# Kernel tuning notes

Hardware: AMD Instinct MI355X
Metric: run time of the kernel (lower is better)

The kernel has to match this reference:

```python
import jax, jax.numpy as jnp
import numpy as np

N = 50000          # nodes
E = 800000         # edges (before self-loops)
F_IN = 500         # input features
H1, C1 = 8, 16     # layer-1 heads, per-head channels
NUM_CLASSES = 7
NEG_SLOPE = 0.2


def setup_inputs() -> dict:
    key = jax.random.key(0)
    ks = jax.random.split(key, 10)
    s = 0.05
    return {
        "x": jax.random.normal(ks[0], (N, F_IN), jnp.float32),
        "edge_index": jax.random.randint(ks[1], (2, E), 0, N, dtype=jnp.int64),
        "W1": jax.random.normal(ks[2], (F_IN, H1 * C1), jnp.float32) * s,
        "att_src1": jax.random.normal(ks[3], (H1, C1), jnp.float32) * s,
        "att_dst1": jax.random.normal(ks[4], (H1, C1), jnp.float32) * s,
        "b1": jnp.zeros((H1 * C1,), jnp.float32),
        "W2": jax.random.normal(ks[5], (H1 * C1, NUM_CLASSES), jnp.float32) * s,
        "att_src2": jax.random.normal(ks[6], (1, NUM_CLASSES), jnp.float32) * s,
        "att_dst2": jax.random.normal(ks[7], (1, NUM_CLASSES), jnp.float32) * s,
        "b2": jnp.zeros((NUM_CLASSES,), jnp.float32),
    }


def _gat_conv(x, W, att_src, att_dst, bias, src, dst, concat):
    # PyG GATConv (eval mode: attention dropout is identity).
    H, C = att_src.shape
    h = (x @ W).reshape(N, H, C)                      # [N,H,C]
    a_src = jnp.sum(h * att_src, axis=-1)             # [N,H]
    a_dst = jnp.sum(h * att_dst, axis=-1)             # [N,H]
    e = a_src[src] + a_dst[dst]                       # [Et,H] per-edge logits
    e = jax.nn.leaky_relu(e, NEG_SLOPE)
    # segment softmax over incoming edges of each destination node
    m = jax.ops.segment_max(e, dst, num_segments=N)   # [N,H]
    e = jnp.exp(e - m[dst])
    denom = jax.ops.segment_sum(e, dst, num_segments=N)  # [N,H]
    alpha = e / (denom[dst] + 1e-16)                  # [Et,H]
    msg = h[src] * alpha[:, :, None]                  # [Et,H,C]
    out = jax.ops.segment_sum(msg, dst, num_segments=N)  # [N,H,C]
    if concat:
        out = out.reshape(N, H * C)
    else:
        out = out.mean(axis=1)
    return out + bias


def reference(x, edge_index, W1, att_src1, att_dst1, b1, W2, att_src2, att_dst2, b2):
    # add self-loops (PyG default add_self_loops=True)
    loops = jnp.arange(N, dtype=edge_index.dtype)
    src = jnp.concatenate([edge_index[0], loops])
    dst = jnp.concatenate([edge_index[1], loops])
    h = _gat_conv(x, W1, att_src1, att_dst1, b1, src, dst, concat=True)
    h = jax.nn.relu(h)
    # F.dropout(p=0.6, training=False) -> identity in eval mode
    out = _gat_conv(h, W2, att_src2, att_dst2, b2, src, dst, concat=False)
    return out
```

## Files before the change

kernel.cpp:

```cpp
#include <hip/hip_runtime.h>
#include <hip/hip_bf16.h>

#define NN 50000
#define EE 800000
#define ETOT 850000
#define FIN 500
#define HC 128
#define NH 8
#define CH 16
#define NC 7

#define OW1  0
#define OAS1 64000
#define OAD1 64128
#define OB1  64256
#define OW2  64384
#define OAS2 65280
#define OAD2 65287
#define OB2  65294
#define WTOT 65301

#define GR1  64
#define GK   32
#define KPAD 512
#define ASTR 40
#define BSTR 40

typedef __hip_bfloat16 bf16;
typedef __attribute__((ext_vector_type(8))) short short8;
typedef __attribute__((ext_vector_type(4))) float f32x4;

__device__ __forceinline__ float b2f(const bf16 v) { return __bfloat162float(v); }
__device__ __forceinline__ float lrelu(float v) { return fmaxf(v, 0.2f * v); }
__device__ __forceinline__ float elog(float v) { return __expf(fminf(lrelu(v), 30.f)); }
__device__ __forceinline__ float blo(unsigned w) { return __uint_as_float(w << 16); }
__device__ __forceinline__ float bhi(unsigned w) { return __uint_as_float(w & 0xffff0000u); }
__device__ __forceinline__ unsigned short f2bu(float f)
{
    bf16 h = __float2bfloat16(f);
    return *(unsigned short*)&h;
}

__device__ __forceinline__ int eread(const void* __restrict__ eidx, long long i, int is64)
{
    if (is64) return (int)((const long long*)eidx)[i];
    return ((const int*)eidx)[i];
}

__global__ void detect_kernel(const unsigned short* __restrict__ xraw,
                              const unsigned int* __restrict__ eraw,
                              int* __restrict__ flags, int* __restrict__ rowptr)
{
    __shared__ int s_insane, s_oddnz;
    if (threadIdx.x == 0) { s_insane = 0; s_oddnz = 0; }
    __syncthreads();
    int insane = 0;
    for (int i = threadIdx.x; i < 8192; i += 256) {
        const unsigned int bits = ((unsigned int)xraw[i]) << 16;
        const float v = __uint_as_float(bits);
        const float a = fabsf(v);
        const bool sane = (v == 0.0f) || (a >= 1e-30f && a <= 1e4f);
        if (!sane) insane++;
    }
    int oddnz = 0;
    for (int i = threadIdx.x; i < 512; i += 256) {
        if (eraw[2 * i + 1] != 0u) oddnz++;
    }
    atomicAdd(&s_insane, insane);
    atomicAdd(&s_oddnz, oddnz);
    __syncthreads();
    if (threadIdx.x == 0) {
        flags[0] = (s_insane < 256) ? 1 : 0;
        flags[1] = (s_oddnz == 0) ? 1 : 0;
        rowptr[NN] = ETOT;
    }
}

__global__ void conv_w_kernel(const void* W1, const void* as1, const void* ad1, const void* b1,
                              const void* W2, const void* as2, const void* ad2, const void* b2,
                              float* __restrict__ wc, const int* __restrict__ flags)
{
    const int i = blockIdx.x * blockDim.x + threadIdx.x;
    if (i >= WTOT) return;
    const void* src; int off;
    if (i < OAS1)      { src = W1;  off = i - OW1; }
    else if (i < OAD1) { src = as1; off = i - OAS1; }
    else if (i < OB1)  { src = ad1; off = i - OAD1; }
    else if (i < OW2)  { src = b1;  off = i - OB1; }
    else if (i < OAS2) { src = W2;  off = i - OW2; }
    else if (i < OAD2) { src = as2; off = i - OAS2; }
    else if (i < OB2)  { src = ad2; off = i - OAD2; }
    else               { src = b2;  off = i - OB2; }
    float v;
    if (flags[0]) v = b2f(((const bf16*)src)[off]);
    else          v = ((const float*)src)[off];
    wc[i] = v;
}

__global__ void conv_w1t_kernel(const void* __restrict__ W1, unsigned short* __restrict__ w1t,
                                const int* __restrict__ flags)
{
    const int i = blockIdx.x * blockDim.x + threadIdx.x;
    if (i >= HC * KPAD) return;
    const int col = i >> 9;
    const int k   = i & (KPAD - 1);
    float v = 0.f;
    if (k < FIN) {
        if (flags[0]) v = b2f(((const bf16*)W1)[k * HC + col]);
        else          v = ((const float*)W1)[k * HC + col];
    }
    w1t[i] = f2bu(v);
}

__global__ void hist_kernel(const void* __restrict__ eidx, int* __restrict__ deg,
                            int* __restrict__ rank, const int* __restrict__ flags)
{
    const int e = blockIdx.x * blockDim.x + threadIdx.x;
    if (e >= ETOT) return;
    int d;
    if (e < EE) d = eread(eidx, (long long)EE + e, flags[1]);
    else        d = e - EE;
    int r = -1;
    if ((unsigned)d < (unsigned)NN) r = atomicAdd(&deg[d], 1);
    rank[e] = r;
}

__global__ void scan_k1_kernel(const int* __restrict__ deg, int* __restrict__ bsum)
{
    __shared__ int lds[256];
    const int i = blockIdx.x * 256 + threadIdx.x;
    lds[threadIdx.x] = (i < NN) ? deg[i] : 0;
    __syncthreads();
    for (int s = 128; s > 0; s >>= 1) {
        if (threadIdx.x < s) lds[threadIdx.x] += lds[threadIdx.x + s];
        __syncthreads();
    }
    if (threadIdx.x == 0) bsum[blockIdx.x] = lds[0];
}

__global__ void scan_k2_kernel(int* __restrict__ bsum)
{
    __shared__ int a[256], b[256], orig[256];
    const int t = threadIdx.x;
    a[t] = bsum[t]; orig[t] = a[t];
    __syncthreads();
    int* cur = a; int* nxt = b;
    for (int off = 1; off < 256; off <<= 1) {
        nxt[t] = cur[t] + ((t >= off) ? cur[t - off] : 0);
        __syncthreads();
        int* tmp = cur; cur = nxt; nxt = tmp;
    }
    bsum[t] = cur[t] - orig[t];
}

__global__ void scan_k3_kernel(const int* __restrict__ deg, const int* __restrict__ bsum,
                               int* __restrict__ rowptr)
{
    __shared__ int a[256], b[256], own[256];
    const int t = threadIdx.x;
    const int i = blockIdx.x * 256 + t;
    const int v = (i < NN) ? deg[i] : 0;
    a[t] = v; own[t] = v;
    __syncthreads();
    int* cur = a; int* nxt = b;
    for (int off = 1; off < 256; off <<= 1) {
        nxt[t] = cur[t] + ((t >= off) ? cur[t - off] : 0);
        __syncthreads();
        int* tmp = cur; cur = nxt; nxt = tmp;
    }
    if (i < NN) rowptr[i] = bsum[blockIdx.x] + cur[t] - own[t];
}

__global__ void scatter_kernel(const void* __restrict__ eidx, const int* __restrict__ rowptr,
                               const int* __restrict__ rank, int* __restrict__ esrc_sorted,
                               const int* __restrict__ flags)
{
    const int e = blockIdx.x * blockDim.x + threadIdx.x;
    if (e >= ETOT) return;
    int s, d;
    if (e < EE) {
        s = eread(eidx, e, flags[1]);
        d = eread(eidx, (long long)EE + e, flags[1]);
    } else s = d = e - EE;
    if ((unsigned)s >= (unsigned)NN || (unsigned)d >= (unsigned)NN) return;
    const int r = rank[e];
    if (r < 0) return;
    const int pos = rowptr[d] + r;
    if ((unsigned)pos < (unsigned)ETOT) esrc_sorted[pos] = s;
}

__global__ __launch_bounds__(256) void gemm1_mfma_kernel(
    const void* __restrict__ x, const unsigned short* __restrict__ w1t,
    bf16* __restrict__ h1, const int* __restrict__ flags)
{
    __shared__ unsigned short Asl[GR1 * ASTR];
    __shared__ unsigned short Bsl[HC * BSTR];

    const int t    = threadIdx.x;
    const int wv   = t >> 6;
    const int lane = t & 63;
    const int m15  = lane & 15;
    const int quad = lane >> 4;
    const int r0   = blockIdx.x * GR1;
    const int isbf = flags[0];
    const float* xf = (const float*)x;
    const bf16*  xb = (const bf16*)x;

    const int wr  = (wv >> 1) * 32;
    const int wcb = (wv & 1) * 64;

    f32x4 acc[2][4];
#pragma unroll
    for (int i = 0; i < 2; ++i)
#pragma unroll
        for (int j = 0; j < 4; ++j) acc[i][j] = (f32x4){0.f, 0.f, 0.f, 0.f};

    const int arow = t >> 2;
    const int akk  = (t & 3) * 8;
    const int bcol = t & 127;
    const int bks  = (t >> 7) * 16;

    for (int kt = 0; kt < 16; ++kt) {
        const int k0 = kt * GK;
        {
            const int grow = r0 + arow;
            if (!isbf && grow < NN && (k0 + akk + 8) <= FIN) {
                const size_t base = (size_t)grow * FIN + k0 + akk;
                const float4 v0 = *(const float4*)(xf + base);
                const float4 v1 = *(const float4*)(xf + base + 4);
                uint4 pk;
                pk.x = (unsigned)f2bu(v0.x) | ((unsigned)f2bu(v0.y) << 16);
                pk.y = (unsigned)f2bu(v0.z) | ((unsigned)f2bu(v0.w) << 16);
                pk.z = (unsigned)f2bu(v1.x) | ((unsigned)f2bu(v1.y) << 16);
                pk.w = (unsigned)f2bu(v1.z) | ((unsigned)f2bu(v1.w) << 16);
                *(uint4*)&Asl[arow * ASTR + akk] = pk;
            } else {
#pragma unroll
                for (int j = 0; j < 8; ++j) {
                    const int k = k0 + akk + j;
                    float v = 0.f;
                    if (grow < NN && k < FIN)
                        v = isbf ? b2f(xb[(size_t)grow * FIN + k]) : xf[(size_t)grow * FIN + k];
                    Asl[arow * ASTR + akk + j] = f2bu(v);
                }
            }
        }
        {
            const unsigned short* gp = w1t + (size_t)bcol * KPAD + k0 + bks;
            *(uint4*)&Bsl[bcol * BSTR + bks]     = *(const uint4*)gp;
            *(uint4*)&Bsl[bcol * BSTR + bks + 8] = *(const uint4*)(gp + 8);
        }
        __syncthreads();

        const int ak = quad * 8;
        const short8 a0 = *(const short8*)&Asl[(wr + m15) * ASTR + ak];
        const short8 a1 = *(const short8*)&Asl[(wr + 16 + m15) * ASTR + ak];
#pragma unroll
        for (int ct = 0; ct < 4; ++ct) {
            const short8 b = *(const short8*)&Bsl[(wcb + ct * 16 + m15) * BSTR + ak];
            acc[0][ct] = __builtin_amdgcn_mfma_f32_16x16x32_bf16(a0, b, acc[0][ct], 0, 0, 0);
            acc[1][ct] = __builtin_amdgcn_mfma_f32_16x16x32_bf16(a1, b, acc[1][ct], 0, 0, 0);
        }
        __syncthreads();
    }

#pragma unroll
    for (int rt = 0; rt < 2; ++rt) {
#pragma unroll
        for (int reg = 0; reg < 4; ++reg) {
            const int row = r0 + wr + rt * 16 + quad * 4 + reg;
            if (row < NN) {
                bf16* hp = h1 + (size_t)row * HC;
#pragma unroll
                for (int ct = 0; ct < 4; ++ct)
                    hp[wcb + ct * 16 + m15] = __float2bfloat16(acc[rt][ct][reg]);
            }
        }
    }
}

__global__ void att1_kernel(const bf16* __restrict__ h1, const float* __restrict__ wc,
                            float* __restrict__ a_src, float* __restrict__ a_dst)
{
    const int idx = blockIdx.x * blockDim.x + threadIdx.x;
    if (idx >= NN * NH) return;
    const int h = idx & 7;
    const unsigned int* hp = (const unsigned int*)(h1 + (size_t)(idx >> 3) * HC + h * CH);
    float s = 0.f, d = 0.f;
#pragma unroll
    for (int u = 0; u < 8; ++u) {
        const unsigned int w = hp[u];
        s += blo(w) * wc[OAS1 + h * CH + 2 * u] + bhi(w) * wc[OAS1 + h * CH + 2 * u + 1];
        d += blo(w) * wc[OAD1 + h * CH + 2 * u] + bhi(w) * wc[OAD1 + h * CH + 2 * u + 1];
    }
    a_src[idx] = s;
    a_dst[idx] = d;
}

__global__ __launch_bounds__(256) void gather1_kernel(
    const int* __restrict__ rowptr, const int* __restrict__ esrc_sorted,
    const float* __restrict__ a_src, const float* __restrict__ a_dst,
    const bf16* __restrict__ h1, float* __restrict__ out1)
{
    const int node = blockIdx.x * 4 + (threadIdx.x >> 6);
    if (node >= NN) return;
    const int lane = threadIdx.x & 63;
    const int h = lane >> 3;
    const float ad = a_dst[node * NH + h];
    const int start = rowptr[node];
    const int end   = rowptr[node + 1];
    float acc0 = 0.f, acc1 = 0.f, den = 0.f;
    int i = start;
    for (; i + 8 <= end; i += 8) {
        int   sv[8];
        float ev[8];
        unsigned wv[8];
#pragma unroll
        for (int j = 0; j < 8; ++j) sv[j] = esrc_sorted[i + j];
#pragma unroll
        for (int j = 0; j < 8; ++j) ev[j] = a_src[sv[j] * NH + h];
#pragma unroll
        for (int j = 0; j < 8; ++j) wv[j] = *(const unsigned*)(h1 + (size_t)sv[j] * HC + 2 * lane);
#pragma unroll
        for (int j = 0; j < 8; ++j) {
            const float n = elog(ev[j] + ad);
            acc0 += n * blo(wv[j]);
            acc1 += n * bhi(wv[j]);
            den  += n;
        }
    }
    for (; i < end; ++i) {
        const int s = esrc_sorted[i];
        const float num = elog(a_src[s * NH + h] + ad);
        const unsigned w = *(const unsigned*)(h1 + (size_t)s * HC + 2 * lane);
        acc0 += num * blo(w);
        acc1 += num * bhi(w);
        den  += num;
    }
    const float inv = 1.f / (den + 1e-16f);
    float* op = out1 + (size_t)node * HC + 2 * lane;
    op[0] = acc0 * inv;
    op[1] = acc1 * inv;
}

__global__ __launch_bounds__(256) void gemm2_kernel(
    const float* __restrict__ out1, const float* __restrict__ wc, float* __restrict__ h2,
    float* __restrict__ a_src2, float* __restrict__ a_dst2)
{
    __shared__ float W2s[HC * NC];
    __shared__ float B1s[HC];
    for (int i = threadIdx.x; i < HC * NC; i += 256) W2s[i] = wc[OW2 + i];
    if (threadIdx.x < HC) B1s[threadIdx.x] = wc[OB1 + threadIdx.x];
    __syncthreads();
    const int nl = threadIdx.x >> 3;
    const int c  = threadIdx.x & 7;
    const int node = blockIdx.x * 32 + nl;
    const bool valid = (node < NN) && (c < NC);
    float acc = 0.f;
    if (valid) {
        const float* hp = out1 + (size_t)node * HC;
#pragma unroll
        for (int k4 = 0; k4 < 32; ++k4) {
            const float4 hv = *(const float4*)&hp[4 * k4];
            acc += fmaxf(hv.x + B1s[4 * k4 + 0], 0.f) * W2s[(4 * k4 + 0) * NC + c];
            acc += fmaxf(hv.y + B1s[4 * k4 + 1], 0.f) * W2s[(4 * k4 + 1) * NC + c];
            acc += fmaxf(hv.z + B1s[4 * k4 + 2], 0.f) * W2s[(4 * k4 + 2) * NC + c];
            acc += fmaxf(hv.w + B1s[4 * k4 + 3], 0.f) * W2s[(4 * k4 + 3) * NC + c];
        }
        h2[node * NC + c] = acc;
    }
    float ps = valid ? acc * wc[OAS2 + c] : 0.f;
    float pd = valid ? acc * wc[OAD2 + c] : 0.f;
#pragma unroll
    for (int m = 1; m < 8; m <<= 1) {
        ps += __shfl_xor(ps, m, 8);
        pd += __shfl_xor(pd, m, 8);
    }
    if (node < NN && c == 0) {
        a_src2[node] = ps;
        a_dst2[node] = pd;
    }
}

__global__ __launch_bounds__(256) void gather2_kernel(
    const int* __restrict__ rowptr, const int* __restrict__ esrc_sorted,
    const float* __restrict__ a_src, const float* __restrict__ a_dst,
    const float* __restrict__ h2, const float* __restrict__ wc,
    void* __restrict__ out, const int* __restrict__ flags)
{
    const int node = blockIdx.x * 32 + (threadIdx.x >> 3);
    if (node >= NN) return;
    const int c = threadIdx.x & 7;
    const float ad = a_dst[node];
    const int start = rowptr[node];
    const int end   = rowptr[node + 1];
    const int cc = (c < NC) ? c : 0;
    float acc = 0.f, den = 0.f;
    int i = start;
    for (; i + 4 <= end; i += 4) {
        const int s0 = esrc_sorted[i + 0];
        const int s1 = esrc_sorted[i + 1];
        const int s2 = esrc_sorted[i + 2];
        const int s3 = esrc_sorted[i + 3];
        const float e0 = a_src[s0];
        const float e1 = a_src[s1];
        const float e2 = a_src[s2];
        const float e3 = a_src[s3];
        const float v0 = h2[s0 * NC + cc];
        const float v1 = h2[s1 * NC + cc];
        const float v2 = h2[s2 * NC + cc];
        const float v3 = h2[s3 * NC + cc];
        const float n0 = elog(e0 + ad);
        const float n1 = elog(e1 + ad);
        const float n2 = elog(e2 + ad);
        const float n3 = elog(e3 + ad);
        acc += n0 * v0 + n1 * v1 + n2 * v2 + n3 * v3;
        den += n0 + n1 + n2 + n3;
    }
    for (; i < end; ++i) {
        const int s = esrc_sorted[i];
        const float num = elog(a_src[s] + ad);
        den += num;
        acc += num * h2[s * NC + cc];
    }
    if (c >= NC) return;
    const float v = acc / (den + 1e-16f) + wc[OB2 + c];
    if (flags[0]) ((bf16*)out)[node * NC + c] = __float2bfloat16(v);
    else          ((float*)out)[node * NC + c] = v;
}

extern "C" void kernel_launch(void* const* d_in, const int* in_sizes, int n_in,
                              void* d_out, int out_size, void* d_ws, size_t ws_size,
                              hipStream_t stream)
{
    const void* x        = d_in[0];
    const void* eidx     = d_in[1];
    const void* W1       = d_in[2];
    const void* att_src1 = d_in[3];
    const void* att_dst1 = d_in[4];
    const void* b1       = d_in[5];
    const void* W2       = d_in[6];
    const void* att_src2 = d_in[7];
    const void* att_dst2 = d_in[8];
    const void* b2       = d_in[9];

    float* ws = (float*)d_ws;
    size_t o = 0;
    int*   flags  = (int*)(ws + o);            o += 16;
    float* wc     = ws + o;                    o += 65312;
    unsigned short* w1t = (unsigned short*)(ws + o); o += (HC * KPAD) / 2;
    int*   deg    = (int*)(ws + o);            o += 50000;
    int*   rowptr = (int*)(ws + o);            o += 50016;
    int*   bsum   = (int*)(ws + o);            o += 256;
    int*   esrt   = (int*)(ws + o);            o += 850000;
    int*   rank   = (int*)(ws + o);            o += 850000;
    bf16*  h1     = (bf16*)(ws + o);           o += (size_t)NN * HC / 2;
    float* a_src1 = ws + o;                    o += (size_t)NN * NH;
    float* a_dst1 = ws + o;                    o += (size_t)NN * NH;
    float* out1   = ws + o;                    o += (size_t)NN * HC;
    float* h2     = ws + o;                    o += (size_t)NN * NC;
    float* a_src2 = ws + o;                    o += NN;
    float* a_dst2 = ws + o;                    o += NN;

    detect_kernel<<<1, 256, 0, stream>>>((const unsigned short*)x, (const unsigned int*)eidx,
                                         flags, rowptr);
    conv_w_kernel<<<(WTOT + 255) / 256, 256, 0, stream>>>(W1, att_src1, att_dst1, b1,
                                                          W2, att_src2, att_dst2, b2, wc, flags);
    conv_w1t_kernel<<<(HC * KPAD + 255) / 256, 256, 0, stream>>>(W1, w1t, flags);
    hipMemsetAsync(deg, 0, (size_t)NN * sizeof(int), stream);
    hist_kernel<<<(ETOT + 255) / 256, 256, 0, stream>>>(eidx, deg, rank, flags);
    scan_k1_kernel<<<(NN + 255) / 256, 256, 0, stream>>>(deg, bsum);
    scan_k2_kernel<<<1, 256, 0, stream>>>(bsum);
    scan_k3_kernel<<<(NN + 255) / 256, 256, 0, stream>>>(deg, bsum, rowptr);
    scatter_kernel<<<(ETOT + 255) / 256, 256, 0, stream>>>(eidx, rowptr, rank, esrt, flags);

    gemm1_mfma_kernel<<<(NN + GR1 - 1) / GR1, 256, 0, stream>>>(x, w1t, h1, flags);
    att1_kernel<<<(NN * NH + 255) / 256, 256, 0, stream>>>(h1, wc, a_src1, a_dst1);
    gather1_kernel<<<(NN + 3) / 4, 256, 0, stream>>>(rowptr, esrt, a_src1, a_dst1, h1, out1);
    gemm2_kernel<<<(NN + 31) / 32, 256, 0, stream>>>(out1, wc, h2, a_src2, a_dst2);
    gather2_kernel<<<(NN + 31) / 32, 256, 0, stream>>>(rowptr, esrt, a_src2, a_dst2, h2, wc, d_out, flags);
}
```

Measured before the change: 340.0 us.

## Fuse attention logits into GEMM1, layer-2 GEMM into gather1, merge weight conversion

The layer-1 attention logits are now computed in the GEMM1 epilogue using cross-lane shuffles, which removes the att1 pass that re-read h1. The layer-2 projection, with bias and ReLU, is fused into gather1, so the fp32 out1 intermediate is never written or re-read. The two weight-conversion kernels are merged into one. The rank array is dropped in favour of a second atomic cursor in scatter, and int64 edge reads now take only the low 32-bit word. Together these cut launches and memory traffic, at the cost of extra shuffles and atomics and a non-deterministic order of edges within each destination.

```diff
diff --git a/kernel.cpp b/kernel.cpp
--- a/kernel.cpp
+++ b/kernel.cpp
@@ -43,7 +43,7 @@
 
 __device__ __forceinline__ int eread(const void* __restrict__ eidx, long long i, int is64)
 {
-    if (is64) return (int)((const long long*)eidx)[i];
+    if (is64) return ((const int*)eidx)[2 * i];
     return ((const int*)eidx)[i];
 }
 
@@ -76,53 +76,49 @@
     }
 }
 
-__global__ void conv_w_kernel(const void* W1, const void* as1, const void* ad1, const void* b1,
-                              const void* W2, const void* as2, const void* ad2, const void* b2,
-                              float* __restrict__ wc, const int* __restrict__ flags)
+__global__ void conv_all_kernel(const void* W1, const void* as1, const void* ad1, const void* b1,
+                                const void* W2, const void* as2, const void* ad2, const void* b2,
+                                float* __restrict__ wc, unsigned short* __restrict__ w1t,
+                                const int* __restrict__ flags)
 {
     const int i = blockIdx.x * blockDim.x + threadIdx.x;
-    if (i >= WTOT) return;
-    const void* src; int off;
-    if (i < OAS1)      { src = W1;  off = i - OW1; }
-    else if (i < OAD1) { src = as1; off = i - OAS1; }
-    else if (i < OB1)  { src = ad1; off = i - OAD1; }
-    else if (i < OW2)  { src = b1;  off = i - OB1; }
-    else if (i < OAS2) { src = W2;  off = i - OW2; }
-    else if (i < OAD2) { src = as2; off = i - OAS2; }
-    else if (i < OB2)  { src = ad2; off = i - OAD2; }
-    else               { src = b2;  off = i - OB2; }
-    float v;
-    if (flags[0]) v = b2f(((const bf16*)src)[off]);
-    else          v = ((const float*)src)[off];
-    wc[i] = v;
-}
-
-__global__ void conv_w1t_kernel(const void* __restrict__ W1, unsigned short* __restrict__ w1t,
-                                const int* __restrict__ flags)
-{
-    const int i = blockIdx.x * blockDim.x + threadIdx.x;
-    if (i >= HC * KPAD) return;
-    const int col = i >> 9;
-    const int k   = i & (KPAD - 1);
-    float v = 0.f;
-    if (k < FIN) {
-        if (flags[0]) v = b2f(((const bf16*)W1)[k * HC + col]);
-        else          v = ((const float*)W1)[k * HC + col];
-    }
-    w1t[i] = f2bu(v);
+    const int isbf = flags[0];
+    if (i < WTOT) {
+        const void* src; int off;
+        if (i < OAS1)      { src = W1;  off = i - OW1; }
+        else if (i < OAD1) { src = as1; off = i - OAS1; }
+        else if (i < OB1)  { src = ad1; off = i - OAD1; }
+        else if (i < OW2)  { src = b1;  off = i - OB1; }
+        else if (i < OAS2) { src = W2;  off = i - OW2; }
+        else if (i < OAD2) { src = as2; off = i - OAS2; }
+        else if (i < OB2)  { src = ad2; off = i - OAD2; }
+        else               { src = b2;  off = i - OB2; }
+        float v;
+        if (isbf) v = b2f(((const bf16*)src)[off]);
+        else      v = ((const float*)src)[off];
+        wc[i] = v;
+    }
+    if (i < HC * KPAD) {
+        const int col = i >> 9;
+        const int k   = i & (KPAD - 1);
+        float v = 0.f;
+        if (k < FIN) {
+            if (isbf) v = b2f(((const bf16*)W1)[k * HC + col]);
+            else      v = ((const float*)W1)[k * HC + col];
+        }
+        w1t[i] = f2bu(v);
+    }
 }
 
 __global__ void hist_kernel(const void* __restrict__ eidx, int* __restrict__ deg,
-                            int* __restrict__ rank, const int* __restrict__ flags)
+                            const int* __restrict__ flags)
 {
     const int e = blockIdx.x * blockDim.x + threadIdx.x;
     if (e >= ETOT) return;
     int d;
     if (e < EE) d = eread(eidx, (long long)EE + e, flags[1]);
     else        d = e - EE;
-    int r = -1;
-    if ((unsigned)d < (unsigned)NN) r = atomicAdd(&deg[d], 1);
-    rank[e] = r;
+    if ((unsigned)d < (unsigned)NN) atomicAdd(&deg[d], 1);
 }
 
 __global__ void scan_k1_kernel(const int* __restrict__ deg, int* __restrict__ bsum)
@@ -172,7 +168,7 @@
 }
 
 __global__ void scatter_kernel(const void* __restrict__ eidx, const int* __restrict__ rowptr,
-                               const int* __restrict__ rank, int* __restrict__ esrc_sorted,
+                               int* __restrict__ cur, int* __restrict__ esrc_sorted,
                                const int* __restrict__ flags)
 {
     const int e = blockIdx.x * blockDim.x + threadIdx.x;
@@ -183,15 +179,15 @@
         d = eread(eidx, (long long)EE + e, flags[1]);
     } else s = d = e - EE;
     if ((unsigned)s >= (unsigned)NN || (unsigned)d >= (unsigned)NN) return;
-    const int r = rank[e];
-    if (r < 0) return;
-    const int pos = rowptr[d] + r;
+    const int pos = rowptr[d] + atomicAdd(&cur[d], 1);
     if ((unsigned)pos < (unsigned)ETOT) esrc_sorted[pos] = s;
 }
 
 __global__ __launch_bounds__(256) void gemm1_mfma_kernel(
     const void* __restrict__ x, const unsigned short* __restrict__ w1t,
-    bf16* __restrict__ h1, const int* __restrict__ flags)
+    bf16* __restrict__ h1, const float* __restrict__ wc,
+    float* __restrict__ a_src1, float* __restrict__ a_dst1,
+    const int* __restrict__ flags)
 {
     __shared__ unsigned short Asl[GR1 * ASTR];
     __shared__ unsigned short Bsl[HC * BSTR];
@@ -264,44 +260,51 @@
         __syncthreads();
     }
 
+    const int hc0 = wcb >> 4;
+    float asw[4], adw[4];
+#pragma unroll
+    for (int ct = 0; ct < 4; ++ct) {
+        asw[ct] = wc[OAS1 + (hc0 + ct) * CH + m15];
+        adw[ct] = wc[OAD1 + (hc0 + ct) * CH + m15];
+    }
 #pragma unroll
     for (int rt = 0; rt < 2; ++rt) {
 #pragma unroll
         for (int reg = 0; reg < 4; ++reg) {
             const int row = r0 + wr + rt * 16 + quad * 4 + reg;
-            if (row < NN) {
-                bf16* hp = h1 + (size_t)row * HC;
-#pragma unroll
-                for (int ct = 0; ct < 4; ++ct)
-                    hp[wcb + ct * 16 + m15] = __float2bfloat16(acc[rt][ct][reg]);
+            const bool ok = (row < NN);
+            bf16* hp = h1 + (size_t)row * HC;
+#pragma unroll
+            for (int ct = 0; ct < 4; ++ct) {
+                const float v = acc[rt][ct][reg];
+                if (ok) hp[wcb + ct * 16 + m15] = __float2bfloat16(v);
+                float s = v * asw[ct];
+                float d = v * adw[ct];
+                s += __shfl_xor(s, 1);  d += __shfl_xor(d, 1);
+                s += __shfl_xor(s, 2);  d += __shfl_xor(d, 2);
+                s += __shfl_xor(s, 4);  d += __shfl_xor(d, 4);
+                s += __shfl_xor(s, 8);  d += __shfl_xor(d, 8);
+                if (ok && m15 == 0) {
+                    a_src1[row * NH + hc0 + ct] = s;
+                    a_dst1[row * NH + hc0 + ct] = d;
+                }
             }
         }
     }
-}
-
-__global__ void att1_kernel(const bf16* __restrict__ h1, const float* __restrict__ wc,
-                            float* __restrict__ a_src, float* __restrict__ a_dst)
-{
-    const int idx = blockIdx.x * blockDim.x + threadIdx.x;
-    if (idx >= NN * NH) return;
-    const int h = idx & 7;
-    const unsigned int* hp = (const unsigned int*)(h1 + (size_t)(idx >> 3) * HC + h * CH);
-    float s = 0.f, d = 0.f;
-#pragma unroll
-    for (int u = 0; u < 8; ++u) {
-        const unsigned int w = hp[u];
-        s += blo(w) * wc[OAS1 + h * CH + 2 * u] + bhi(w) * wc[OAS1 + h * CH + 2 * u + 1];
-        d += blo(w) * wc[OAD1 + h * CH + 2 * u] + bhi(w) * wc[OAD1 + h * CH + 2 * u + 1];
-    }
-    a_src[idx] = s;
-    a_dst[idx] = d;
 }
 
 __global__ __launch_bounds__(256) void gather1_kernel(
     const int* __restrict__ rowptr, const int* __restrict__ esrc_sorted,
     const float* __restrict__ a_src, const float* __restrict__ a_dst,
-    const bf16* __restrict__ h1, float* __restrict__ out1)
-{
+    const bf16* __restrict__ h1, const float* __restrict__ wc,
+    float* __restrict__ h2, float* __restrict__ a_src2, float* __restrict__ a_dst2)
+{
+    __shared__ float W2s[HC * NC];
+    __shared__ float B1s[HC];
+    for (int i = threadIdx.x; i < HC * NC; i += 256) W2s[i] = wc[OW2 + i];
+    if (threadIdx.x < HC) B1s[threadIdx.x] = wc[OB1 + threadIdx.x];
+    __syncthreads();
+
     const int node = blockIdx.x * 4 + (threadIdx.x >> 6);
     if (node >= NN) return;
     const int lane = threadIdx.x & 63;
@@ -338,51 +341,34 @@
         den  += num;
     }
     const float inv = 1.f / (den + 1e-16f);
-    float* op = out1 + (size_t)node * HC + 2 * lane;
-    op[0] = acc0 * inv;
-    op[1] = acc1 * inv;
-}
-
-__global__ __launch_bounds__(256) void gemm2_kernel(
-    const float* __restrict__ out1, const float* __restrict__ wc, float* __restrict__ h2,
-    float* __restrict__ a_src2, float* __restrict__ a_dst2)
-{
-    __shared__ float W2s[HC * NC];
-    __shared__ float B1s[HC];
-    for (int i = threadIdx.x; i < HC * NC; i += 256) W2s[i] = wc[OW2 + i];
-    if (threadIdx.x < HC) B1s[threadIdx.x] = wc[OB1 + threadIdx.x];
-    __syncthreads();
-    const int nl = threadIdx.x >> 3;
-    const int c  = threadIdx.x & 7;
-    const int node = blockIdx.x * 32 + nl;
-    const bool valid = (node < NN) && (c < NC);
-    float acc = 0.f;
-    if (valid) {
-        const float* hp = out1 + (size_t)node * HC;
-#pragma unroll
-        for (int k4 = 0; k4 < 32; ++k4) {
-            const float4 hv = *(const float4*)&hp[4 * k4];
-            acc += fmaxf(hv.x + B1s[4 * k4 + 0], 0.f) * W2s[(4 * k4 + 0) * NC + c];
-            acc += fmaxf(hv.y + B1s[4 * k4 + 1], 0.f) * W2s[(4 * k4 + 1) * NC + c];
-            acc += fmaxf(hv.z + B1s[4 * k4 + 2], 0.f) * W2s[(4 * k4 + 2) * NC + c];
-            acc += fmaxf(hv.w + B1s[4 * k4 + 3], 0.f) * W2s[(4 * k4 + 3) * NC + c];
-        }
-        h2[node * NC + c] = acc;
-    }
-    float ps = valid ? acc * wc[OAS2 + c] : 0.f;
-    float pd = valid ? acc * wc[OAD2 + c] : 0.f;
-#pragma unroll
-    for (int m = 1; m < 8; m <<= 1) {
-        ps += __shfl_xor(ps, m, 8);
-        pd += __shfl_xor(pd, m, 8);
-    }
-    if (node < NN && c == 0) {
+
+    const int k0 = 2 * lane;
+    const float r0v = fmaxf(acc0 * inv + B1s[k0],     0.f);
+    const float r1v = fmaxf(acc1 * inv + B1s[k0 + 1], 0.f);
+    float p[NC];
+#pragma unroll
+    for (int c = 0; c < NC; ++c)
+        p[c] = r0v * W2s[k0 * NC + c] + r1v * W2s[(k0 + 1) * NC + c];
+#pragma unroll
+    for (int m = 1; m < 64; m <<= 1) {
+#pragma unroll
+        for (int c = 0; c < NC; ++c) p[c] += __shfl_xor(p[c], m);
+    }
+    if (lane == 0) {
+        float ps = 0.f, pd = 0.f;
+        float* hp = h2 + (size_t)node * NC;
+#pragma unroll
+        for (int c = 0; c < NC; ++c) {
+            hp[c] = p[c];
+            ps += p[c] * wc[OAS2 + c];
+            pd += p[c] * wc[OAD2 + c];
+        }
         a_src2[node] = ps;
         a_dst2[node] = pd;
     }
 }
 
-__global__ __launch_bounds__(256) void gather2_kernel(
+__global__ void gather2_kernel(
     const int* __restrict__ rowptr, const int* __restrict__ esrc_sorted,
     const float* __restrict__ a_src, const float* __restrict__ a_dst,
     const float* __restrict__ h2, const float* __restrict__ wc,
@@ -450,33 +436,32 @@
     float* wc     = ws + o;                    o += 65312;
     unsigned short* w1t = (unsigned short*)(ws + o); o += (HC * KPAD) / 2;
     int*   deg    = (int*)(ws + o);            o += 50000;
+    int*   cur    = (int*)(ws + o);            o += 50000;
     int*   rowptr = (int*)(ws + o);            o += 50016;
     int*   bsum   = (int*)(ws + o);            o += 256;
     int*   esrt   = (int*)(ws + o);            o += 850000;
-    int*   rank   = (int*)(ws + o);            o += 850000;
     bf16*  h1     = (bf16*)(ws + o);           o += (size_t)NN * HC / 2;
     float* a_src1 = ws + o;                    o += (size_t)NN * NH;
     float* a_dst1 = ws + o;                    o += (size_t)NN * NH;
-    float* out1   = ws + o;                    o += (size_t)NN * HC;
     float* h2     = ws + o;                    o += (size_t)NN * NC;
     float* a_src2 = ws + o;                    o += NN;
     float* a_dst2 = ws + o;                    o += NN;
 
     detect_kernel<<<1, 256, 0, stream>>>((const unsigned short*)x, (const unsigned int*)eidx,
                                          flags, rowptr);
-    conv_w_kernel<<<(WTOT + 255) / 256, 256, 0, stream>>>(W1, att_src1, att_dst1, b1,
-                                                          W2, att_src2, att_dst2, b2, wc, flags);
-    conv_w1t_kernel<<<(HC * KPAD + 255) / 256, 256, 0, stream>>>(W1, w1t, flags);
-    hipMemsetAsync(deg, 0, (size_t)NN * sizeof(int), stream);
-    hist_kernel<<<(ETOT + 255) / 256, 256, 0, stream>>>(eidx, deg, rank, flags);
+    conv_all_kernel<<<(HC * KPAD + 255) / 256, 256, 0, stream>>>(
+        W1, att_src1, att_dst1, b1, W2, att_src2, att_dst2, b2, wc, w1t, flags);
+    hipMemsetAsync(deg, 0, 2 * (size_t)NN * sizeof(int), stream);
+    hist_kernel<<<(ETOT + 255) / 256, 256, 0, stream>>>(eidx, deg, flags);
     scan_k1_kernel<<<(NN + 255) / 256, 256, 0, stream>>>(deg, bsum);
     scan_k2_kernel<<<1, 256, 0, stream>>>(bsum);
     scan_k3_kernel<<<(NN + 255) / 256, 256, 0, stream>>>(deg, bsum, rowptr);
-    scatter_kernel<<<(ETOT + 255) / 256, 256, 0, stream>>>(eidx, rowptr, rank, esrt, flags);
-
-    gemm1_mfma_kernel<<<(NN + GR1 - 1) / GR1, 256, 0, stream>>>(x, w1t, h1, flags);
-    att1_kernel<<<(NN * NH + 255) / 256, 256, 0, stream>>>(h1, wc, a_src1, a_dst1);
-    gather1_kernel<<<(NN + 3) / 4, 256, 0, stream>>>(rowptr, esrt, a_src1, a_dst1, h1, out1);
-    gemm2_kernel<<<(NN + 31) / 32, 256, 0, stream>>>(out1, wc, h2, a_src2, a_dst2);
-    gather2_kernel<<<(NN + 31) / 32, 256, 0, stream>>>(rowptr, esrt, a_src2, a_dst2, h2, wc, d_out, flags);
-}
+    scatter_kernel<<<(ETOT + 255) / 256, 256, 0, stream>>>(eidx, rowptr, cur, esrt, flags);
+
+    gemm1_mfma_kernel<<<(NN + GR1 - 1) / GR1, 256, 0, stream>>>(x, w1t, h1, wc,
+                                                                a_src1, a_dst1, flags);
+    gather1_kernel<<<(NN + 3) / 4, 256, 0, stream>>>(rowptr, esrt, a_src1, a_dst1, h1, wc,
+                                                     h2, a_src2, a_dst2);
+    gather2_kernel<<<(NN + 31) / 32, 256, 0, stream>>>(rowptr, esrt, a_src2, a_dst2, h2, wc,
+                                                       d_out, flags);
+}
```

After: 368.6 us. 1.08x slower.
